# Performance work log

Measured on AMD Instinct MI355X. Metric: run time of the kernel, lower is better.

The kernel has to match this reference:

```python
import jax, jax.numpy as jnp
import numpy as np

N_USERS = 50000
N_ENTITIES = 100000
N_NODES = N_USERS + N_ENTITIES
N_EDGES = 3000000
EMB_DIM = 64
WEIGHT_SIZES = [64, 64, 32, 16]  # [emb_dim] + weight_size
BATCH = 8192
LEAKY_SLOPE = 0.2  # KGAT (TF reference) uses leaky_relu alpha=0.2
EPS = 1e-12


def setup_inputs() -> dict:
    key = jax.random.key(0)
    ks = jax.random.split(key, 24)
    inp = {}
    inp["users"] = jax.random.randint(ks[0], (BATCH,), 0, N_USERS, dtype=jnp.int32)
    inp["pos_items"] = jax.random.randint(ks[1], (BATCH,), 0, N_ENTITIES, dtype=jnp.int32)
    inp["neg_items"] = jax.random.randint(ks[2], (BATCH,), 0, N_ENTITIES, dtype=jnp.int32)
    inp["all_h"] = jax.random.randint(ks[3], (N_EDGES,), 0, N_NODES, dtype=jnp.int32)
    inp["all_t"] = jax.random.randint(ks[4], (N_EDGES,), 0, N_NODES, dtype=jnp.int32)
    inp["A_values"] = jax.random.uniform(ks[5], (N_EDGES,), dtype=jnp.float32)
    inp["user_embed"] = jax.random.normal(ks[6], (N_USERS, EMB_DIM), dtype=jnp.float32) * 0.1
    inp["entity_embed"] = jax.random.normal(ks[7], (N_ENTITIES, EMB_DIM), dtype=jnp.float32) * 0.1
    ki = 8
    for k in range(3):
        din, dout = WEIGHT_SIZES[k], WEIGHT_SIZES[k + 1]
        scale = float(np.sqrt(2.0 / (din + dout)))  # xavier-ish
        inp[f"W_gc_{k}"] = jax.random.normal(ks[ki], (din, dout), dtype=jnp.float32) * scale; ki += 1
        inp[f"b_gc_{k}"] = jax.random.normal(ks[ki], (1, dout), dtype=jnp.float32) * scale; ki += 1
        inp[f"W_bi_{k}"] = jax.random.normal(ks[ki], (din, dout), dtype=jnp.float32) * scale; ki += 1
        inp[f"b_bi_{k}"] = jax.random.normal(ks[ki], (1, dout), dtype=jnp.float32) * scale; ki += 1
    return inp


def _bi_interaction(ego, all_h, all_t, A_values, layers, n_nodes):
    # KGAT bi-interaction aggregator over edge-list sparse adjacency.
    outs = [ego]
    for (W_gc, b_gc, W_bi, b_bi) in layers:
        # sparse A @ ego : gather tails, weight by attention, scatter-add to heads
        msgs = A_values[:, None] * ego[all_t]                       # [E, d]
        side = jax.ops.segment_sum(msgs, all_h, num_segments=n_nodes)  # [N, d]
        sum_emb = jax.nn.leaky_relu((ego + side) @ W_gc + b_gc, negative_slope=LEAKY_SLOPE)
        bi_emb = jax.nn.leaky_relu((ego * side) @ W_bi + b_bi, negative_slope=LEAKY_SLOPE)
        ego = sum_emb + bi_emb
        norm = ego / jnp.maximum(jnp.linalg.norm(ego, axis=1, keepdims=True), EPS)
        outs.append(norm)
    return jnp.concatenate(outs, axis=1)  # [N, 64+64+32+16]


def reference(users, pos_items, neg_items, all_h, all_t, A_values,
              user_embed, entity_embed,
              W_gc_0, b_gc_0, W_bi_0, b_bi_0,
              W_gc_1, b_gc_1, W_bi_1, b_bi_1,
              W_gc_2, b_gc_2, W_bi_2, b_bi_2):
    n_users = user_embed.shape[0]
    n_nodes = n_users + entity_embed.shape[0]
    ego = jnp.concatenate([user_embed, entity_embed], axis=0)  # [N, 64]
    layers = [(W_gc_0, b_gc_0, W_bi_0, b_bi_0),
              (W_gc_1, b_gc_1, W_bi_1, b_bi_1),
              (W_gc_2, b_gc_2, W_bi_2, b_bi_2)]
    all_emb = _bi_interaction(ego, all_h, all_t, A_values, layers, n_nodes)
    ua, ea = all_emb[:n_users], all_emb[n_users:]
    u_e = ua[users]
    pos_i_e = ea[pos_items]
    neg_i_e = ea[neg_items]
    return (u_e, pos_i_e, neg_i_e)
```

## Files before the change

### kernel.cpp

```cpp
#include <hip/hip_runtime.h>
#include <math.h>

#define N_USERS    50000
#define N_ENTITIES 100000
#define N_NODES    150000
#define N_EDGES    3000000
#define BATCH      8192
#define SLOPE      0.2f
#define EPSF       1e-12f

#define NBUK   2344
#define CAP    1536
#define BLK_E  8192
#define NPB    ((N_EDGES + BLK_E - 1) / BLK_E)
#define PBLK   1024

__device__ __forceinline__ unsigned f2bf(float f) {
    unsigned u = __float_as_uint(f);
    return (u + 0x7FFFu + ((u >> 16) & 1u)) >> 16;
}
__device__ __forceinline__ float bf_lo(unsigned d) { return __uint_as_float(d << 16); }
__device__ __forceinline__ float bf_hi(unsigned d) { return __uint_as_float(d & 0xFFFF0000u); }

__global__ __launch_bounds__(256)
void cast0_k(const float* __restrict__ user_emb, const float* __restrict__ ent_emb,
             unsigned short* __restrict__ ego0_bf) {
    int idx = blockIdx.x * 256 + threadIdx.x;
    const int total = N_NODES * 64 / 4;
    if (idx >= total) return;
    int ge = idx * 4;
    const float* src = (ge < N_USERS * 64) ? user_emb + ge
                                           : ent_emb + (ge - N_USERS * 64);
    float4 v = *(const float4*)src;
    ushort4 o;
    o.x = (unsigned short)f2bf(v.x);
    o.y = (unsigned short)f2bf(v.y);
    o.z = (unsigned short)f2bf(v.z);
    o.w = (unsigned short)f2bf(v.w);
    *(ushort4*)(ego0_bf + ge) = o;
}

__global__ __launch_bounds__(PBLK)
void partition_k(const int* __restrict__ all_h, const int* __restrict__ all_t,
                 const float* __restrict__ A,
                 int* __restrict__ gcursor, int2* __restrict__ rec) {
    __shared__ int hist[NBUK];
    __shared__ int cnt2[NBUK];
    int t = threadIdx.x;
    for (int i = t; i < NBUK; i += PBLK) { hist[i] = 0; cnt2[i] = 0; }
    __syncthreads();

    int e0 = blockIdx.x * BLK_E;
    int e1 = e0 + BLK_E; if (e1 > N_EDGES) e1 = N_EDGES;

    for (int e = e0 + t; e < e1; e += PBLK)
        atomicAdd(&hist[all_h[e] >> 6], 1);
    __syncthreads();

    for (int i = t; i < NBUK; i += PBLK) {
        int c = hist[i];
        hist[i] = c ? atomicAdd(&gcursor[i], c) : 0;
    }
    __syncthreads();

    for (int e = e0 + t; e < e1; e += PBLK) {
        int h = all_h[e];
        int b = h >> 6;
        int r = hist[b] + atomicAdd(&cnt2[b], 1);
        if (r < CAP)
            rec[(size_t)b * CAP + r] =
                make_int2(all_t[e] | ((h & 63) << 18), __float_as_int(A[e]));
    }
}

__global__ __launch_bounds__(256)
void local_sort_k(const int* __restrict__ gcursor, int2* __restrict__ rec,
                  int2* __restrict__ range) {
    __shared__ int2 sin[CAP];
    __shared__ int2 sout[CAP];
    __shared__ int cnt64[64];
    __shared__ int pos64[64];
    int b = blockIdx.x, t = threadIdx.x;
    int cnt = gcursor[b]; if (cnt > CAP) cnt = CAP;

    if (t < 64) cnt64[t] = 0;
    __syncthreads();

    for (int i = t; i < cnt; i += 256) {
        int2 p = rec[(size_t)b * CAP + i];
        sin[i] = p;
        atomicAdd(&cnt64[(p.x >> 18) & 63], 1);
    }
    __syncthreads();

    if (t < 64) {
        int v = cnt64[t];
        int sum = v;
        #pragma unroll
        for (int off = 1; off < 64; off <<= 1) {
            int x = __shfl_up(sum, off, 64);
            if (t >= off) sum += x;
        }
        pos64[t] = sum - v;
    }
    __syncthreads();

    for (int i = t; i < cnt; i += 256) {
        int2 p = sin[i];
        int l = (p.x >> 18) & 63;
        int dst = atomicAdd(&pos64[l], 1);
        sout[dst] = make_int2(p.x & 0x3FFFF, p.y);
    }
    __syncthreads();

    for (int i = t; i < cnt; i += 256)
        rec[(size_t)b * CAP + i] = sout[i];

    if (t < 64) {
        int v = cnt64[t];
        int sum = v;
        #pragma unroll
        for (int off = 1; off < 64; off <<= 1) {
            int x = __shfl_up(sum, off, 64);
            if (t >= off) sum += x;
        }
        int start = b * CAP + (sum - v);
        int node = b * 64 + t;
        if (node < N_NODES) range[node] = make_int2(start, start + v);
    }
}

template<int DIN>
__global__ __launch_bounds__(256)
void side_k(const int2* __restrict__ range, const int2* __restrict__ rec,
            const unsigned short* __restrict__ tab, float* __restrict__ side) {
    constexpr int LPR = DIN / 8;
    constexpr int EPW = 64 / LPR;

    int w = threadIdx.x >> 6;
    int lane = threadIdx.x & 63;
    int h = blockIdx.x * 4 + w;

    int2 rg = range[h];
    int e0 = rg.x, e1 = rg.y;
    int g = lane / LPR;
    int q = lane % LPR;

    float acc[8];
    #pragma unroll
    for (int j = 0; j < 8; ++j) acc[j] = 0.f;

    for (int e = e0; e < e1; e += 2 * EPW) {
        int i0 = e + g;
        int i1 = e + EPW + g;
        int c0 = i0 < e1 ? i0 : e1 - 1;
        int c1 = i1 < e1 ? i1 : e1 - 1;
        int2 p0 = rec[c0];
        int2 p1 = rec[c1];
        float a0 = (i0 < e1) ? __int_as_float(p0.y) : 0.f;
        float a1 = (i1 < e1) ? __int_as_float(p1.y) : 0.f;
        uint4 d0 = *(const uint4*)(tab + (size_t)p0.x * DIN + q * 8);
        uint4 d1 = *(const uint4*)(tab + (size_t)p1.x * DIN + q * 8);
        acc[0] = fmaf(a0, bf_lo(d0.x), acc[0]);
        acc[1] = fmaf(a0, bf_hi(d0.x), acc[1]);
        acc[2] = fmaf(a0, bf_lo(d0.y), acc[2]);
        acc[3] = fmaf(a0, bf_hi(d0.y), acc[3]);
        acc[4] = fmaf(a0, bf_lo(d0.z), acc[4]);
        acc[5] = fmaf(a0, bf_hi(d0.z), acc[5]);
        acc[6] = fmaf(a0, bf_lo(d0.w), acc[6]);
        acc[7] = fmaf(a0, bf_hi(d0.w), acc[7]);
        acc[0] = fmaf(a1, bf_lo(d1.x), acc[0]);
        acc[1] = fmaf(a1, bf_hi(d1.x), acc[1]);
        acc[2] = fmaf(a1, bf_lo(d1.y), acc[2]);
        acc[3] = fmaf(a1, bf_hi(d1.y), acc[3]);
        acc[4] = fmaf(a1, bf_lo(d1.z), acc[4]);
        acc[5] = fmaf(a1, bf_hi(d1.z), acc[5]);
        acc[6] = fmaf(a1, bf_lo(d1.w), acc[6]);
        acc[7] = fmaf(a1, bf_hi(d1.w), acc[7]);
    }

    #pragma unroll
    for (int off = LPR; off < 64; off <<= 1)
        #pragma unroll
        for (int j = 0; j < 8; ++j) acc[j] += __shfl_xor(acc[j], off, 64);

    if (lane < LPR) {
        float* dst = side + (size_t)h * DIN + q * 8;
        *(float4*)dst       = make_float4(acc[0], acc[1], acc[2], acc[3]);
        *(float4*)(dst + 4) = make_float4(acc[4], acc[5], acc[6], acc[7]);
    }
}

template<int DIN, int DOUT, int TILE_ROWS, bool CONCAT, bool OUT_BF>
__global__ __launch_bounds__(256)
void transform_k(const unsigned short* __restrict__ ego_in,
                 const float* __restrict__ user_emb, const float* __restrict__ ent_emb,
                 const float* __restrict__ side,
                 const float* __restrict__ Wgc, const float* __restrict__ bgc,
                 const float* __restrict__ Wbi, const float* __restrict__ bbi,
                 void* __restrict__ ego_out) {
    constexpr int NG = DOUT / 8;
    constexpr int RG = 256 / NG;
    constexpr int RT = TILE_ROWS / RG;
    constexpr int STRIDE = DIN + 4;
    constexpr int KC8 = DIN / 8;

    __shared__ float sWgc[DIN * DOUT], sWbi[DIN * DOUT];
    __shared__ float sU[TILE_ROWS * STRIDE], sV[TILE_ROWS * STRIDE];

    int t = threadIdx.x;

    for (int i = t * 4; i < DIN * DOUT; i += 1024) {
        *(float4*)&sWgc[i] = *(const float4*)&Wgc[i];
        *(float4*)&sWbi[i] = *(const float4*)&Wbi[i];
    }

    int base = blockIdx.x * TILE_ROWS;
    for (int f = t; f < TILE_ROWS * KC8; f += 256) {
        int row = f / KC8, c8 = f % KC8;
        int n = base + row;
        int nc = n < N_NODES ? n : N_NODES - 1;
        float ev[8];
        if (CONCAT) {
            const float* erow = (nc < N_USERS) ? user_emb + (size_t)nc * 64
                                               : ent_emb + (size_t)(nc - N_USERS) * 64;
            float4 a = *(const float4*)(erow + c8 * 8);
            float4 b = *(const float4*)(erow + c8 * 8 + 4);
            ev[0] = a.x; ev[1] = a.y; ev[2] = a.z; ev[3] = a.w;
            ev[4] = b.x; ev[5] = b.y; ev[6] = b.z; ev[7] = b.w;
        } else {
            uint4 d = *(const uint4*)(ego_in + (size_t)nc * DIN + c8 * 8);
            ev[0] = bf_lo(d.x); ev[1] = bf_hi(d.x);
            ev[2] = bf_lo(d.y); ev[3] = bf_hi(d.y);
            ev[4] = bf_lo(d.z); ev[5] = bf_hi(d.z);
            ev[6] = bf_lo(d.w); ev[7] = bf_hi(d.w);
        }
        const float* srow = side + (size_t)nc * DIN + c8 * 8;
        float4 s0 = *(const float4*)srow;
        float4 s1 = *(const float4*)(srow + 4);
        float sv8[8] = {s0.x, s0.y, s0.z, s0.w, s1.x, s1.y, s1.z, s1.w};
        float* pu = &sU[row * STRIDE + c8 * 8];
        float* pv = &sV[row * STRIDE + c8 * 8];
        *(float4*)pu       = make_float4(ev[0] + sv8[0], ev[1] + sv8[1], ev[2] + sv8[2], ev[3] + sv8[3]);
        *(float4*)(pu + 4) = make_float4(ev[4] + sv8[4], ev[5] + sv8[5], ev[6] + sv8[6], ev[7] + sv8[7]);
        *(float4*)pv       = make_float4(ev[0] * sv8[0], ev[1] * sv8[1], ev[2] * sv8[2], ev[3] * sv8[3]);
        *(float4*)(pv + 4) = make_float4(ev[4] * sv8[4], ev[5] * sv8[5], ev[6] * sv8[6], ev[7] * sv8[7]);
    }
    __syncthreads();

    int cg = t % NG, rgi = t / NG;
    int c0 = cg * 8;
    int r0 = rgi * RT;

    float accg[RT][8], accb[RT][8];
    #pragma unroll
    for (int r = 0; r < RT; ++r)
        #pragma unroll
        for (int j = 0; j < 8; ++j) { accg[r][j] = 0.f; accb[r][j] = 0.f; }

    for (int k = 0; k < DIN; k += 4) {
        float4 u4[RT], v4[RT];
        #pragma unroll
        for (int r = 0; r < RT; ++r) {
            u4[r] = *(const float4*)&sU[(r0 + r) * STRIDE + k];
            v4[r] = *(const float4*)&sV[(r0 + r) * STRIDE + k];
        }
        #pragma unroll
        for (int kk = 0; kk < 4; ++kk) {
            float4 wg0 = *(const float4*)&sWgc[(k + kk) * DOUT + c0];
            float4 wg1 = *(const float4*)&sWgc[(k + kk) * DOUT + c0 + 4];
            float4 wb0 = *(const float4*)&sWbi[(k + kk) * DOUT + c0];
            float4 wb1 = *(const float4*)&sWbi[(k + kk) * DOUT + c0 + 4];
            #pragma unroll
            for (int r = 0; r < RT; ++r) {
                float u = ((const float*)&u4[r])[kk];
                float v = ((const float*)&v4[r])[kk];
                accg[r][0] = fmaf(u, wg0.x, accg[r][0]);
                accg[r][1] = fmaf(u, wg0.y, accg[r][1]);
                accg[r][2] = fmaf(u, wg0.z, accg[r][2]);
                accg[r][3] = fmaf(u, wg0.w, accg[r][3]);
                accg[r][4] = fmaf(u, wg1.x, accg[r][4]);
                accg[r][5] = fmaf(u, wg1.y, accg[r][5]);
                accg[r][6] = fmaf(u, wg1.z, accg[r][6]);
                accg[r][7] = fmaf(u, wg1.w, accg[r][7]);
                accb[r][0] = fmaf(v, wb0.x, accb[r][0]);
                accb[r][1] = fmaf(v, wb0.y, accb[r][1]);
                accb[r][2] = fmaf(v, wb0.z, accb[r][2]);
                accb[r][3] = fmaf(v, wb0.w, accb[r][3]);
                accb[r][4] = fmaf(v, wb1.x, accb[r][4]);
                accb[r][5] = fmaf(v, wb1.y, accb[r][5]);
                accb[r][6] = fmaf(v, wb1.z, accb[r][6]);
                accb[r][7] = fmaf(v, wb1.w, accb[r][7]);
            }
        }
    }

    float4 bg0 = *(const float4*)&bgc[c0];
    float4 bg1 = *(const float4*)&bgc[c0 + 4];
    float4 bb0 = *(const float4*)&bbi[c0];
    float4 bb1 = *(const float4*)&bbi[c0 + 4];
    float bg[8] = {bg0.x, bg0.y, bg0.z, bg0.w, bg1.x, bg1.y, bg1.z, bg1.w};
    float bb[8] = {bb0.x, bb0.y, bb0.z, bb0.w, bb1.x, bb1.y, bb1.z, bb1.w};

    #pragma unroll
    for (int r = 0; r < RT; ++r) {
        int n = base + r0 + r;
        if (n < N_NODES) {
            float o[8];
            #pragma unroll
            for (int j = 0; j < 8; ++j) {
                float gg = accg[r][j] + bg[j];
                float b2 = accb[r][j] + bb[j];
                gg = gg > 0.f ? gg : SLOPE * gg;
                b2 = b2 > 0.f ? b2 : SLOPE * b2;
                o[j] = gg + b2;
            }
            if (OUT_BF) {
                unsigned short* dst = (unsigned short*)ego_out + (size_t)n * DOUT + c0;
                uint4 wv;
                wv.x = f2bf(o[0]) | (f2bf(o[1]) << 16);
                wv.y = f2bf(o[2]) | (f2bf(o[3]) << 16);
                wv.z = f2bf(o[4]) | (f2bf(o[5]) << 16);
                wv.w = f2bf(o[6]) | (f2bf(o[7]) << 16);
                *(uint4*)dst = wv;
            } else {
                float* dst = (float*)ego_out + (size_t)n * DOUT + c0;
                *(float4*)dst       = make_float4(o[0], o[1], o[2], o[3]);
                *(float4*)(dst + 4) = make_float4(o[4], o[5], o[6], o[7]);
            }
        }
    }
}

__global__ __launch_bounds__(64)
void gather_k(const int* __restrict__ users, const int* __restrict__ pos,
              const int* __restrict__ neg,
              const float* __restrict__ user_emb, const float* __restrict__ ent_emb,
              const unsigned short* __restrict__ ego1_bf,
              const unsigned short* __restrict__ ego2_bf,
              const float* __restrict__ ego3,
              float* __restrict__ out) {
    int r = blockIdx.x;
    int lane = threadIdx.x;
    int which = r / BATCH;
    int i = r - which * BATCH;
    int node;
    if (which == 0)      node = users[i];
    else if (which == 1) node = N_USERS + pos[i];
    else                 node = N_USERS + neg[i];

    float* o = out + (size_t)r * 176;

    float x0 = (node < N_USERS) ? user_emb[(size_t)node * 64 + lane]
                                : ent_emb[(size_t)(node - N_USERS) * 64 + lane];
    o[lane] = x0;

    float x1 = __uint_as_float((unsigned)ego1_bf[(size_t)node * 64 + lane] << 16);
    float ss = x1 * x1;
    #pragma unroll
    for (int off = 32; off > 0; off >>= 1) ss += __shfl_xor(ss, off, 64);
    o[64 + lane] = x1 / fmaxf(sqrtf(ss), EPSF);

    float x2 = (lane < 32)
        ? __uint_as_float((unsigned)ego2_bf[(size_t)node * 32 + lane] << 16) : 0.f;
    float ss2 = x2 * x2;
    #pragma unroll
    for (int off = 32; off > 0; off >>= 1) ss2 += __shfl_xor(ss2, off, 64);
    if (lane < 32) o[128 + lane] = x2 / fmaxf(sqrtf(ss2), EPSF);

    float x3 = (lane < 16) ? ego3[(size_t)node * 16 + lane] : 0.f;
    float ss3 = x3 * x3;
    #pragma unroll
    for (int off = 32; off > 0; off >>= 1) ss3 += __shfl_xor(ss3, off, 64);
    if (lane < 16) o[160 + lane] = x3 / fmaxf(sqrtf(ss3), EPSF);
}

extern "C" void kernel_launch(void* const* d_in, const int* in_sizes, int n_in,
                              void* d_out, int out_size, void* d_ws, size_t ws_size,
                              hipStream_t stream) {
    const int*   users    = (const int*)d_in[0];
    const int*   pos      = (const int*)d_in[1];
    const int*   neg      = (const int*)d_in[2];
    const int*   all_h    = (const int*)d_in[3];
    const int*   all_t    = (const int*)d_in[4];
    const float* A        = (const float*)d_in[5];
    const float* user_emb = (const float*)d_in[6];
    const float* ent_emb  = (const float*)d_in[7];
    const float* Wgc0 = (const float*)d_in[8];
    const float* bgc0 = (const float*)d_in[9];
    const float* Wbi0 = (const float*)d_in[10];
    const float* bbi0 = (const float*)d_in[11];
    const float* Wgc1 = (const float*)d_in[12];
    const float* bgc1 = (const float*)d_in[13];
    const float* Wbi1 = (const float*)d_in[14];
    const float* bbi1 = (const float*)d_in[15];
    const float* Wgc2 = (const float*)d_in[16];
    const float* bgc2 = (const float*)d_in[17];
    const float* Wbi2 = (const float*)d_in[18];
    const float* bbi2 = (const float*)d_in[19];

    char* p = (char*)d_ws;
    int*   gcursor = (int*)p;            p += ((size_t)NBUK * 4 + 255) & ~255ull;
    int2*  rec     = (int2*)p;           char* rec_base = p;
    p += ((size_t)NBUK * CAP * 8 + 255) & ~255ull;
    int2*  range   = (int2*)p;           p += ((size_t)N_NODES * 8 + 255) & ~255ull;
    float* side    = (float*)p;          p += ((size_t)N_NODES * 64 * 4 + 255) & ~255ull;
    unsigned short* ego0_bf = (unsigned short*)p; p += ((size_t)N_NODES * 64 * 2 + 255) & ~255ull;
    unsigned short* ego1_bf = (unsigned short*)p; p += ((size_t)N_NODES * 64 * 2 + 255) & ~255ull;
    unsigned short* ego2_bf = (unsigned short*)p; p += ((size_t)N_NODES * 32 * 2 + 255) & ~255ull;
    float* ego3    = (float*)rec_base;
    float* out     = (float*)d_out;

    const int nodeBlocks = N_NODES / 4;

    (void)hipMemsetAsync(gcursor, 0, (size_t)NBUK * 4, stream);
    cast0_k<<<(N_NODES * 64 / 4 + 255) / 256, 256, 0, stream>>>(user_emb, ent_emb, ego0_bf);
    partition_k<<<NPB, PBLK, 0, stream>>>(all_h, all_t, A, gcursor, rec);
    local_sort_k<<<NBUK, 256, 0, stream>>>(gcursor, rec, range);

    side_k<64><<<nodeBlocks, 256, 0, stream>>>(range, rec, ego0_bf, side);
    transform_k<64, 64, 64, true, true><<<(N_NODES + 63) / 64, 256, 0, stream>>>(
        nullptr, user_emb, ent_emb, side, Wgc0, bgc0, Wbi0, bbi0, ego1_bf);

    side_k<64><<<nodeBlocks, 256, 0, stream>>>(range, rec, ego1_bf, side);
    transform_k<64, 32, 64, false, true><<<(N_NODES + 63) / 64, 256, 0, stream>>>(
        ego1_bf, nullptr, nullptr, side, Wgc1, bgc1, Wbi1, bbi1, ego2_bf);

    side_k<32><<<nodeBlocks, 256, 0, stream>>>(range, rec, ego2_bf, side);
    transform_k<32, 16, 128, false, false><<<(N_NODES + 127) / 128, 256, 0, stream>>>(
        ego2_bf, nullptr, nullptr, side, Wgc2, bgc2, Wbi2, bbi2, ego3);

    gather_k<<<3 * BATCH, 64, 0, stream>>>(
        users, pos, neg, user_emb, ent_emb, ego1_bf, ego2_bf, ego3, out);
}
```

Before: 516.2 us.

## Locally sort edges per block before scatter and pad global bucket cursors

Rewrites the partition kernel so each block first builds a bucket histogram, runs a block-wide prefix scan and writes a local permutation in shared memory. Edges are then emitted in bucket order, so consecutive threads write contiguous ranges of the record array instead of scattering at random. The global bucket cursors are spread out with a stride of 16 ints to reduce atomic contention on shared cache lines, and each block now handles more edges. The cost is more shared memory, extra syncs and a second read of the head array per edge.

```diff
diff --git a/kernel.cpp b/kernel.cpp
--- a/kernel.cpp
+++ b/kernel.cpp
@@ -11,9 +11,11 @@
 
 #define NBUK   2344
 #define CAP    1536
-#define BLK_E  8192
+#define BLK_E  12288
 #define NPB    ((N_EDGES + BLK_E - 1) / BLK_E)
 #define PBLK   1024
+#define EPT    (BLK_E / PBLK)
+#define GC_STRIDE 16
 
 __device__ __forceinline__ unsigned f2bf(float f) {
     unsigned u = __float_as_uint(f);
@@ -44,32 +46,82 @@
 void partition_k(const int* __restrict__ all_h, const int* __restrict__ all_t,
                  const float* __restrict__ A,
                  int* __restrict__ gcursor, int2* __restrict__ rec) {
-    __shared__ int hist[NBUK];
-    __shared__ int cnt2[NBUK];
+    __shared__ int pos[NBUK];
+    __shared__ int gbase[NBUK];
+    __shared__ unsigned short perm[BLK_E];
+    __shared__ int wsum[PBLK / 64];
+
     int t = threadIdx.x;
-    for (int i = t; i < NBUK; i += PBLK) { hist[i] = 0; cnt2[i] = 0; }
+    for (int i = t; i < NBUK; i += PBLK) pos[i] = 0;
     __syncthreads();
 
     int e0 = blockIdx.x * BLK_E;
     int e1 = e0 + BLK_E; if (e1 > N_EDGES) e1 = N_EDGES;
 
-    for (int e = e0 + t; e < e1; e += PBLK)
-        atomicAdd(&hist[all_h[e] >> 6], 1);
-    __syncthreads();
-
-    for (int i = t; i < NBUK; i += PBLK) {
-        int c = hist[i];
-        hist[i] = c ? atomicAdd(&gcursor[i], c) : 0;
-    }
-    __syncthreads();
-
-    for (int e = e0 + t; e < e1; e += PBLK) {
-        int h = all_h[e];
-        int b = h >> 6;
-        int r = hist[b] + atomicAdd(&cnt2[b], 1);
-        if (r < CAP)
-            rec[(size_t)b * CAP + r] =
-                make_int2(all_t[e] | ((h & 63) << 18), __float_as_int(A[e]));
+    int h[EPT];
+    #pragma unroll
+    for (int k = 0; k < EPT; ++k) {
+        int e = e0 + k * PBLK + t;
+        h[k] = (e < e1) ? all_h[e] : -1;
+    }
+    #pragma unroll
+    for (int k = 0; k < EPT; ++k)
+        if (h[k] >= 0) atomicAdd(&pos[h[k] >> 6], 1);
+    __syncthreads();
+
+    int c[3];
+    int i0 = t * 3;
+    int tsum = 0;
+    #pragma unroll
+    for (int j = 0; j < 3; ++j) {
+        int idx = i0 + j;
+        c[j] = (idx < NBUK) ? pos[idx] : 0;
+        tsum += c[j];
+        if (idx < NBUK)
+            gbase[idx] = c[j] ? atomicAdd(&gcursor[idx * GC_STRIDE], c[j]) : 0;
+    }
+
+    int lane = t & 63, w = t >> 6;
+    int incl = tsum;
+    #pragma unroll
+    for (int off = 1; off < 64; off <<= 1) {
+        int x = __shfl_up(incl, off, 64);
+        if (lane >= off) incl += x;
+    }
+    if (lane == 63) wsum[w] = incl;
+    __syncthreads();
+    int wbase = 0;
+    for (int j = 0; j < w; ++j) wbase += wsum[j];
+    int excl = wbase + (incl - tsum);
+
+    #pragma unroll
+    for (int j = 0; j < 3; ++j) {
+        int idx = i0 + j;
+        if (idx < NBUK) pos[idx] = excl;
+        excl += c[j];
+    }
+    __syncthreads();
+
+    #pragma unroll
+    for (int k = 0; k < EPT; ++k) {
+        if (h[k] >= 0) {
+            int p = atomicAdd(&pos[h[k] >> 6], 1);
+            perm[p] = (unsigned short)(k * PBLK + t);
+        }
+    }
+    __syncthreads();
+
+    int tot = pos[NBUK - 1];
+    for (int p = t; p < tot; p += PBLK) {
+        int li = perm[p];
+        int e = e0 + li;
+        int hh = all_h[e];
+        int b = hh >> 6;
+        int start = (b > 0) ? pos[b - 1] : 0;
+        int gr = gbase[b] + (p - start);
+        if (gr < CAP)
+            rec[(size_t)b * CAP + gr] =
+                make_int2(all_t[e] | ((hh & 63) << 18), __float_as_int(A[e]));
     }
 }
 
@@ -81,7 +133,7 @@
     __shared__ int cnt64[64];
     __shared__ int pos64[64];
     int b = blockIdx.x, t = threadIdx.x;
-    int cnt = gcursor[b]; if (cnt > CAP) cnt = CAP;
+    int cnt = gcursor[(size_t)b * GC_STRIDE]; if (cnt > CAP) cnt = CAP;
 
     if (t < 64) cnt64[t] = 0;
     __syncthreads();
@@ -400,7 +452,7 @@
     const float* bbi2 = (const float*)d_in[19];
 
     char* p = (char*)d_ws;
-    int*   gcursor = (int*)p;            p += ((size_t)NBUK * 4 + 255) & ~255ull;
+    int*   gcursor = (int*)p;            p += ((size_t)NBUK * GC_STRIDE * 4 + 255) & ~255ull;
     int2*  rec     = (int2*)p;           char* rec_base = p;
     p += ((size_t)NBUK * CAP * 8 + 255) & ~255ull;
     int2*  range   = (int2*)p;           p += ((size_t)N_NODES * 8 + 255) & ~255ull;
@@ -413,7 +465,7 @@
 
     const int nodeBlocks = N_NODES / 4;
 
-    (void)hipMemsetAsync(gcursor, 0, (size_t)NBUK * 4, stream);
+    (void)hipMemsetAsync(gcursor, 0, (size_t)NBUK * GC_STRIDE * 4, stream);
     cast0_k<<<(N_NODES * 64 / 4 + 255) / 256, 256, 0, stream>>>(user_emb, ent_emb, ego0_bf);
     partition_k<<<NPB, PBLK, 0, stream>>>(all_h, all_t, A, gcursor, rec);
     local_sort_k<<<NBUK, 256, 0, stream>>>(gcursor, rec, range);
```

Result: no change. 520.5 us (+0.8%).
